# Kernel tuning notes

Hardware: AMD Instinct MI355X
Metric: run time of the kernel (lower is better)

Reference implementation:

```python
import jax, jax.numpy as jnp
import numpy as np

N = 8192
F_IN = 256
F_OUT = 256


def setup_inputs() -> dict:
    key = jax.random.key(0)
    k1, k2, k3, k4 = jax.random.split(key, 4)
    return {
        "input": jax.random.normal(k1, (N, F_IN), dtype=jnp.float32),
        "adj": jax.random.uniform(k2, (N, N), dtype=jnp.float32),
        "weight": jax.random.normal(k3, (F_IN, F_OUT), dtype=jnp.float32) * (1.0 / np.sqrt(F_OUT)),
        "bias": jax.random.normal(k4, (F_OUT,), dtype=jnp.float32) * (1.0 / np.sqrt(F_OUT)),
    }


def reference(input, adj, weight, bias):
    n = input.shape[0]
    # add_identity=True: adj <- adj + I
    a = adj + jnp.eye(n, dtype=adj.dtype)
    # D^{-1/2} as a vector; diag-matmul == row/col elementwise scaling
    d = jax.lax.rsqrt(jnp.sum(a, axis=1))  # [n]
    adj_norm = d[:, None] * a * d[None, :]  # [n, n]
    support = input @ weight                # [n, f_out]
    out = adj_norm @ support + bias         # [n, f_out]
    return out
```

## Files before the change

kernel.cpp:

```cpp
#include <hip/hip_runtime.h>
#include <stdint.h>

#define N_ROWS 8192
#define F_DIM 256

typedef __attribute__((ext_vector_type(8))) short s16x8;
typedef __attribute__((ext_vector_type(4))) float f32x4;
typedef __attribute__((address_space(3))) uint32_t lds_u32_t;
typedef __attribute__((address_space(1))) const uint32_t gbl_u32_t;

__device__ __forceinline__ void gl_lds16(const void* g, void* l) {
    __builtin_amdgcn_global_load_lds((gbl_u32_t*)g, (lds_u32_t*)l, 16, 0, 0);
}

__device__ __forceinline__ unsigned short f2bf(float f) {
    unsigned int u = __float_as_uint(f);
    u += 0x7FFFu + ((u >> 16) & 1u);
    return (unsigned short)(u >> 16);
}
__device__ __forceinline__ float bf2f(unsigned short h) {
    return __uint_as_float(((unsigned int)h) << 16);
}
__device__ __forceinline__ s16x8 cvt8(f32x4 a, f32x4 b) {
    s16x8 r;
    r[0] = (short)f2bf(a[0]); r[1] = (short)f2bf(a[1]);
    r[2] = (short)f2bf(a[2]); r[3] = (short)f2bf(a[3]);
    r[4] = (short)f2bf(b[0]); r[5] = (short)f2bf(b[1]);
    r[6] = (short)f2bf(b[2]); r[7] = (short)f2bf(b[3]);
    return r;
}

__global__ void k_rowsum(const float* __restrict__ adj, float* __restrict__ dvec) {
    const int row = blockIdx.x;
    const float4* p = (const float4*)(adj + (size_t)row * N_ROWS);
    float s = 0.f;
#pragma unroll
    for (int i = 0; i < 8; ++i) {
        float4 v = p[threadIdx.x + i * 256];
        s += (v.x + v.y) + (v.z + v.w);
    }
#pragma unroll
    for (int off = 32; off > 0; off >>= 1) s += __shfl_down(s, off, 64);
    __shared__ float red[4];
    if ((threadIdx.x & 63) == 0) red[threadIdx.x >> 6] = s;
    __syncthreads();
    if (threadIdx.x == 0) {
        float t = red[0] + red[1] + red[2] + red[3] + 1.0f;
        dvec[row] = rsqrtf(t);
    }
}

__global__ void k_wt(const float* __restrict__ w, unsigned short* __restrict__ wt) {
    const int j = blockIdx.x, t = threadIdx.x;
    wt[j * F_DIM + t] = f2bf(w[t * F_DIM + j]);
}

__global__ __launch_bounds__(256, 2)
void k_support(const float* __restrict__ input, const unsigned short* __restrict__ wt,
               const float* __restrict__ dvec, unsigned short* __restrict__ sup) {
    __shared__ float As[128 * 32];
    __shared__ unsigned short Bs[128 * 32];
    const int tid = threadIdx.x, lane = tid & 63, wid = tid >> 6;
    const int wm = wid & 1, wn = wid >> 1;
    const int l15 = lane & 15, q4 = lane >> 4;
    const int m0 = blockIdx.x * 128, n0 = blockIdx.y * 128;

    uint32_t aoff[4], alds[4], boff[2], blds[2];
#pragma unroll
    for (int i = 0; i < 4; ++i) {
        int row = wid * 32 + i * 8 + (lane >> 3);
        aoff[i] = (uint32_t)(m0 + row) * F_DIM + (lane & 7) * 4;
        alds[i] = (uint32_t)(wid * 32 + i * 8) * 32;
    }
#pragma unroll
    for (int i = 0; i < 2; ++i) {
        int row = wid * 32 + i * 16 + (lane >> 2);
        boff[i] = (uint32_t)(n0 + row) * F_DIM + (lane & 3) * 8;
        blds[i] = (uint32_t)(wid * 32 + i * 16) * 32;
    }

    const f32x4* aptr[4];
    const s16x8* bptr[4];
#pragma unroll
    for (int a = 0; a < 4; ++a)
        aptr[a] = (const f32x4*)(As + (wm * 64 + a * 16 + l15) * 32 + q4 * 8);
#pragma unroll
    for (int b = 0; b < 4; ++b)
        bptr[b] = (const s16x8*)(Bs + (wn * 64 + b * 16 + l15) * 32 + q4 * 8);

    f32x4 acc[4][4];
#pragma unroll
    for (int a = 0; a < 4; ++a)
#pragma unroll
        for (int b = 0; b < 4; ++b) acc[a][b] = (f32x4){0.f, 0.f, 0.f, 0.f};

#pragma unroll 1
    for (int it = 0; it < F_DIM / 32; ++it) {
        __syncthreads();
#pragma unroll
        for (int i = 0; i < 4; ++i) gl_lds16(input + aoff[i], As + alds[i]);
#pragma unroll
        for (int i = 0; i < 2; ++i) gl_lds16(wt + boff[i], Bs + blds[i]);
        __syncthreads();
        s16x8 af[4];
#pragma unroll
        for (int a = 0; a < 4; ++a) af[a] = cvt8(aptr[a][0], aptr[a][1]);
#pragma unroll
        for (int b = 0; b < 4; ++b) {
            s16x8 bf = *bptr[b];
#pragma unroll
            for (int a = 0; a < 4; ++a)
                acc[a][b] = __builtin_amdgcn_mfma_f32_16x16x32_bf16(af[a], bf, acc[a][b], 0, 0, 0);
        }
#pragma unroll
        for (int i = 0; i < 4; ++i) aoff[i] += 32;
#pragma unroll
        for (int i = 0; i < 2; ++i) boff[i] += 32;
    }

#pragma unroll
    for (int a = 0; a < 4; ++a) {
        const int rbase = m0 + wm * 64 + a * 16 + q4 * 4;
        float dv[4];
#pragma unroll
        for (int r = 0; r < 4; ++r) dv[r] = dvec[rbase + r];
#pragma unroll
        for (int b = 0; b < 4; ++b) {
            const int col = n0 + wn * 64 + b * 16 + l15;
            f32x4 c = acc[a][b];
#pragma unroll
            for (int r = 0; r < 4; ++r)
                sup[(size_t)(rbase + r) * F_DIM + col] = f2bf(dv[r] * c[r]);
        }
    }
}

__global__ void k_transpose(const unsigned short* __restrict__ src,
                            unsigned short* __restrict__ dst) {
    __shared__ unsigned short t[64][65];
    const int r0 = blockIdx.x * 64, c0 = blockIdx.y * 64;
    const int lr = threadIdx.x >> 2, lc = (threadIdx.x & 3) * 16;
#pragma unroll
    for (int i = 0; i < 16; ++i)
        t[lr][lc + i] = src[(size_t)(r0 + lr) * F_DIM + c0 + lc + i];
    __syncthreads();
#pragma unroll
    for (int i = 0; i < 16; ++i)
        dst[(size_t)(c0 + lr) * N_ROWS + r0 + lc + i] = t[lc + i][lr];
}

__global__ __launch_bounds__(256, 2)
void k_main(const float* __restrict__ adj, const unsigned short* __restrict__ sup_t,
            const unsigned short* __restrict__ sup, const float* __restrict__ dvec,
            const float* __restrict__ bias, float* __restrict__ out) {
    __shared__ float As[128 * 32];
    __shared__ unsigned short Bs[256 * 32];
    const int tid = threadIdx.x, lane = tid & 63, wid = tid >> 6;
    const int wm = wid & 1, wn = wid >> 1;
    const int l15 = lane & 15, q4 = lane >> 4;
    const int m0 = blockIdx.x * 128;
    const int kbase = blockIdx.y * (N_ROWS / 8);

    uint32_t aoff[4], alds[4], boff[4], blds[4];
#pragma unroll
    for (int i = 0; i < 4; ++i) {
        int arow = wid * 32 + i * 8 + (lane >> 3);
        aoff[i] = (uint32_t)(m0 + arow) * N_ROWS + kbase + (lane & 7) * 4;
        alds[i] = (uint32_t)(wid * 32 + i * 8) * 32;
        int brow = wid * 64 + i * 16 + (lane >> 2);
        boff[i] = (uint32_t)brow * N_ROWS + kbase + (lane & 3) * 8;
        blds[i] = (uint32_t)(wid * 64 + i * 16) * 32;
    }

    const f32x4* aptr[4];
    const s16x8* bptr[8];
#pragma unroll
    for (int a = 0; a < 4; ++a)
        aptr[a] = (const f32x4*)(As + (wm * 64 + a * 16 + l15) * 32 + q4 * 8);
#pragma unroll
    for (int b = 0; b < 8; ++b)
        bptr[b] = (const s16x8*)(Bs + (wn * 128 + b * 16 + l15) * 32 + q4 * 8);

    f32x4 acc[4][8];
#pragma unroll
    for (int a = 0; a < 4; ++a)
#pragma unroll
        for (int b = 0; b < 8; ++b) acc[a][b] = (f32x4){0.f, 0.f, 0.f, 0.f};

#pragma unroll 1
    for (int it = 0; it < (N_ROWS / 8) / 32; ++it) {
        __syncthreads();
#pragma unroll
        for (int i = 0; i < 4; ++i) gl_lds16(adj + aoff[i], As + alds[i]);
#pragma unroll
        for (int i = 0; i < 4; ++i) gl_lds16(sup_t + boff[i], Bs + blds[i]);
        __syncthreads();
        s16x8 af[4];
#pragma unroll
        for (int a = 0; a < 4; ++a) af[a] = cvt8(aptr[a][0], aptr[a][1]);
#pragma unroll
        for (int b = 0; b < 8; ++b) {
            s16x8 bf = *bptr[b];
#pragma unroll
            for (int a = 0; a < 4; ++a)
                acc[a][b] = __builtin_amdgcn_mfma_f32_16x16x32_bf16(af[a], bf, acc[a][b], 0, 0, 0);
        }
#pragma unroll
        for (int i = 0; i < 4; ++i) { aoff[i] += 32; boff[i] += 32; }
    }

    const bool first = (blockIdx.y == 0);
#pragma unroll
    for (int a = 0; a < 4; ++a) {
        const int rbase = m0 + wm * 64 + a * 16 + q4 * 4;
        float dv[4];
#pragma unroll
        for (int r = 0; r < 4; ++r) dv[r] = dvec[rbase + r];
#pragma unroll
        for (int b = 0; b < 8; ++b) {
            const int col = wn * 128 + b * 16 + l15;
            f32x4 c = acc[a][b];
            float bb = first ? bias[col] : 0.f;
#pragma unroll
            for (int r = 0; r < 4; ++r) {
                float v = dv[r] * c[r];
                if (first)
                    v += dv[r] * bf2f(sup[(size_t)(rbase + r) * F_DIM + col]) + bb;
                atomicAdd(out + (size_t)(rbase + r) * F_DIM + col, v);
            }
        }
    }
}

extern "C" void kernel_launch(void* const* d_in, const int* in_sizes, int n_in,
                              void* d_out, int out_size, void* d_ws, size_t ws_size,
                              hipStream_t stream) {
    const float* input  = (const float*)d_in[0];
    const float* adj    = (const float*)d_in[1];
    const float* weight = (const float*)d_in[2];
    const float* bias   = (const float*)d_in[3];
    float* out = (float*)d_out;

    char* ws = (char*)d_ws;
    float* dvec           = (float*)ws;
    unsigned short* wt    = (unsigned short*)(ws + (32 << 10));
    unsigned short* sup   = (unsigned short*)(ws + (32 << 10) + (128 << 10));
    unsigned short* sup_t = (unsigned short*)(ws + (32 << 10) + (128 << 10)
                                              + (size_t)N_ROWS * F_DIM * 2);

    hipMemsetAsync(d_out, 0, (size_t)N_ROWS * F_DIM * sizeof(float), stream);
    k_rowsum<<<dim3(N_ROWS), dim3(256), 0, stream>>>(adj, dvec);
    k_wt<<<dim3(F_DIM), dim3(F_DIM), 0, stream>>>(weight, wt);
    k_support<<<dim3(64, 2), dim3(256), 0, stream>>>(input, wt, dvec, sup);
    k_transpose<<<dim3(128, 4), dim3(256), 0, stream>>>(sup, sup_t);
    k_main<<<dim3(64, 8), dim3(256), 0, stream>>>(adj, sup_t, sup, dvec, bias, out);
}
```

Measured before the change: 516.8 us.

## Replace atomic split-K with partial buffers and separate reduce kernel

The main GEMM tile shrinks from 128 to 64 rows per block and split-K drops from 8 to 4 strips. Each block now writes its partial sums to a per-split workspace buffer instead of issuing float atomics into the output. A new reduce kernel sums the partials and applies the row scaling, the identity term and the bias, so the output memset is no longer needed. This removes atomic traffic and the memset, at the cost of an extra 32 MB partial write and read, another kernel launch, and lower B-tile reuse per block.

```diff
diff --git a/kernel.cpp b/kernel.cpp
--- a/kernel.cpp
+++ b/kernel.cpp
@@ -3,6 +3,8 @@
 
 #define N_ROWS 8192
 #define F_DIM 256
+#define SPLITK 4
+#define KSTRIP (N_ROWS / SPLITK)
 
 typedef __attribute__((ext_vector_type(8))) short s16x8;
 typedef __attribute__((ext_vector_type(4))) float f32x4;
@@ -151,85 +153,101 @@
 
 __global__ __launch_bounds__(256, 2)
 void k_main(const float* __restrict__ adj, const unsigned short* __restrict__ sup_t,
-            const unsigned short* __restrict__ sup, const float* __restrict__ dvec,
-            const float* __restrict__ bias, float* __restrict__ out) {
-    __shared__ float As[128 * 32];
+            float* __restrict__ part) {
+    __shared__ float As[64 * 32];
     __shared__ unsigned short Bs[256 * 32];
     const int tid = threadIdx.x, lane = tid & 63, wid = tid >> 6;
-    const int wm = wid & 1, wn = wid >> 1;
     const int l15 = lane & 15, q4 = lane >> 4;
-    const int m0 = blockIdx.x * 128;
-    const int kbase = blockIdx.y * (N_ROWS / 8);
-
-    uint32_t aoff[4], alds[4], boff[4], blds[4];
-#pragma unroll
-    for (int i = 0; i < 4; ++i) {
-        int arow = wid * 32 + i * 8 + (lane >> 3);
-        aoff[i] = (uint32_t)(m0 + arow) * N_ROWS + kbase + (lane & 7) * 4;
-        alds[i] = (uint32_t)(wid * 32 + i * 8) * 32;
-        int brow = wid * 64 + i * 16 + (lane >> 2);
-        boff[i] = (uint32_t)brow * N_ROWS + kbase + (lane & 3) * 8;
-        blds[i] = (uint32_t)(wid * 64 + i * 16) * 32;
+    const int m0 = blockIdx.x * 64;
+    const int kbase = blockIdx.y * KSTRIP;
+
+    uint32_t aoff[2], alds[2];
+#pragma unroll
+    for (int r = 0; r < 2; ++r) {
+        int idx = r * 256 + tid;
+        aoff[r] = (uint32_t)(m0 + (idx >> 3)) * N_ROWS + kbase + (idx & 7) * 4;
+        alds[r] = (uint32_t)(r * 1024 + wid * 256);
+    }
+    uint32_t boff[4], blds[4];
+#pragma unroll
+    for (int r = 0; r < 4; ++r) {
+        int idx = r * 256 + tid;
+        boff[r] = (uint32_t)(idx >> 2) * N_ROWS + kbase + (idx & 3) * 8;
+        blds[r] = (uint32_t)(r * 2048 + wid * 512);
     }
 
     const f32x4* aptr[4];
-    const s16x8* bptr[8];
-#pragma unroll
-    for (int a = 0; a < 4; ++a)
-        aptr[a] = (const f32x4*)(As + (wm * 64 + a * 16 + l15) * 32 + q4 * 8);
-#pragma unroll
-    for (int b = 0; b < 8; ++b)
-        bptr[b] = (const s16x8*)(Bs + (wn * 128 + b * 16 + l15) * 32 + q4 * 8);
-
-    f32x4 acc[4][8];
-#pragma unroll
-    for (int a = 0; a < 4; ++a)
-#pragma unroll
-        for (int b = 0; b < 8; ++b) acc[a][b] = (f32x4){0.f, 0.f, 0.f, 0.f};
+    const s16x8* bptr[4];
+#pragma unroll
+    for (int a = 0; a < 4; ++a)
+        aptr[a] = (const f32x4*)(As + (a * 16 + l15) * 32 + q4 * 8);
+#pragma unroll
+    for (int b = 0; b < 4; ++b)
+        bptr[b] = (const s16x8*)(Bs + (wid * 64 + b * 16 + l15) * 32 + q4 * 8);
+
+    f32x4 acc[4][4];
+#pragma unroll
+    for (int a = 0; a < 4; ++a)
+#pragma unroll
+        for (int b = 0; b < 4; ++b) acc[a][b] = (f32x4){0.f, 0.f, 0.f, 0.f};
 
 #pragma unroll 1
-    for (int it = 0; it < (N_ROWS / 8) / 32; ++it) {
-        __syncthreads();
-#pragma unroll
-        for (int i = 0; i < 4; ++i) gl_lds16(adj + aoff[i], As + alds[i]);
-#pragma unroll
-        for (int i = 0; i < 4; ++i) gl_lds16(sup_t + boff[i], Bs + blds[i]);
+    for (int it = 0; it < KSTRIP / 32; ++it) {
+        __syncthreads();
+#pragma unroll
+        for (int r = 0; r < 2; ++r) gl_lds16(adj + aoff[r], As + alds[r]);
+#pragma unroll
+        for (int r = 0; r < 4; ++r) gl_lds16(sup_t + boff[r], Bs + blds[r]);
         __syncthreads();
         s16x8 af[4];
 #pragma unroll
         for (int a = 0; a < 4; ++a) af[a] = cvt8(aptr[a][0], aptr[a][1]);
 #pragma unroll
-        for (int b = 0; b < 8; ++b) {
+        for (int b = 0; b < 4; ++b) {
             s16x8 bf = *bptr[b];
 #pragma unroll
             for (int a = 0; a < 4; ++a)
                 acc[a][b] = __builtin_amdgcn_mfma_f32_16x16x32_bf16(af[a], bf, acc[a][b], 0, 0, 0);
         }
 #pragma unroll
-        for (int i = 0; i < 4; ++i) { aoff[i] += 32; boff[i] += 32; }
-    }
-
-    const bool first = (blockIdx.y == 0);
+        for (int r = 0; r < 2; ++r) aoff[r] += 32;
+#pragma unroll
+        for (int r = 0; r < 4; ++r) boff[r] += 32;
+    }
+
+    float* p = part + (size_t)blockIdx.y * ((size_t)N_ROWS * F_DIM);
 #pragma unroll
     for (int a = 0; a < 4; ++a) {
-        const int rbase = m0 + wm * 64 + a * 16 + q4 * 4;
-        float dv[4];
-#pragma unroll
-        for (int r = 0; r < 4; ++r) dv[r] = dvec[rbase + r];
-#pragma unroll
-        for (int b = 0; b < 8; ++b) {
-            const int col = wn * 128 + b * 16 + l15;
+        const int rbase = m0 + a * 16 + q4 * 4;
+#pragma unroll
+        for (int b = 0; b < 4; ++b) {
+            const int col = wid * 64 + b * 16 + l15;
             f32x4 c = acc[a][b];
-            float bb = first ? bias[col] : 0.f;
-#pragma unroll
-            for (int r = 0; r < 4; ++r) {
-                float v = dv[r] * c[r];
-                if (first)
-                    v += dv[r] * bf2f(sup[(size_t)(rbase + r) * F_DIM + col]) + bb;
-                atomicAdd(out + (size_t)(rbase + r) * F_DIM + col, v);
-            }
-        }
-    }
+#pragma unroll
+            for (int r = 0; r < 4; ++r)
+                p[(size_t)(rbase + r) * F_DIM + col] = c[r];
+        }
+    }
+}
+
+__global__ void k_reduce(const float* __restrict__ part, const unsigned short* __restrict__ sup,
+                         const float* __restrict__ dvec, const float* __restrict__ bias,
+                         float* __restrict__ out) {
+    const int gid = blockIdx.x * 256 + threadIdx.x;
+    const int row = gid >> 6;
+    const int c = (gid & 63) * 4;
+    const size_t off = (size_t)row * F_DIM + c;
+    const size_t PS = (size_t)N_ROWS * F_DIM;
+    f32x4 v = *(const f32x4*)(part + off);
+#pragma unroll
+    for (int s = 1; s < SPLITK; ++s) v += *(const f32x4*)(part + s * PS + off);
+    const float d = dvec[row];
+    const unsigned short* sp = sup + off;
+    const f32x4 bb = *(const f32x4*)(bias + c);
+    f32x4 o;
+#pragma unroll
+    for (int r = 0; r < 4; ++r) o[r] = d * (v[r] + bf2f(sp[r])) + bb[r];
+    *(f32x4*)(out + off) = o;
 }
 
 extern "C" void kernel_launch(void* const* d_in, const int* in_sizes, int n_in,
@@ -247,11 +265,13 @@
     unsigned short* sup   = (unsigned short*)(ws + (32 << 10) + (128 << 10));
     unsigned short* sup_t = (unsigned short*)(ws + (32 << 10) + (128 << 10)
                                               + (size_t)N_ROWS * F_DIM * 2);
-
-    hipMemsetAsync(d_out, 0, (size_t)N_ROWS * F_DIM * sizeof(float), stream);
+    float* part           = (float*)(ws + (32 << 10) + (128 << 10)
+                                     + 2 * (size_t)N_ROWS * F_DIM * 2);
+
     k_rowsum<<<dim3(N_ROWS), dim3(256), 0, stream>>>(adj, dvec);
     k_wt<<<dim3(F_DIM), dim3(F_DIM), 0, stream>>>(weight, wt);
     k_support<<<dim3(64, 2), dim3(256), 0, stream>>>(input, wt, dvec, sup);
     k_transpose<<<dim3(128, 4), dim3(256), 0, stream>>>(sup, sup_t);
-    k_main<<<dim3(64, 8), dim3(256), 0, stream>>>(adj, sup_t, sup, dvec, bias, out);
-}
+    k_main<<<dim3(128, SPLITK), dim3(256), 0, stream>>>(adj, sup_t, part);
+    k_reduce<<<dim3((N_ROWS * F_DIM / 4) / 256), dim3(256), 0, stream>>>(part, sup, dvec, bias, out);
+}
```

New measurement: 485.3 us. -6.1%, faster.
